# Kernel optimization log

Hardware: AMD Instinct MI355X
Metric: run time of the kernel (lower is better)

Reference implementation:

```python
import jax, jax.numpy as jnp
import numpy as np

DIM = 2048
NUM_EXPERTS = 64
TOP_K = 2


def setup_inputs() -> dict:
    key = jax.random.key(0)
    kx, kw = jax.random.split(key)
    x = jax.random.normal(kx, (4, 8192, DIM), dtype=jnp.float32)
    # nn.Linear(dim, num_experts, bias=False) -> weight [num_experts, dim]
    W = jax.random.normal(kw, (NUM_EXPERTS, DIM), dtype=jnp.float32) * (1.0 / np.sqrt(DIM))
    return {"x": x, "W": W}


def reference(x, W):
    # gate scores: [B, S, E]
    gate_scores = jnp.einsum("bsd,ed->bse", x, W)
    # top-k over experts
    top_k_values, top_k_indices = jax.lax.top_k(gate_scores, TOP_K)
    top_k_weights = jax.nn.softmax(top_k_values, axis=-1)  # [B, S, K]
    # load-balancing aux loss
    expert_usage = jax.nn.softmax(gate_scores, axis=-1).mean(axis=(0, 1))  # [E]
    aux_loss = NUM_EXPERTS * jnp.sum(expert_usage ** 2)
    return (top_k_indices, top_k_weights, aux_loss)
```

## Files before the change

kernel.cpp:

```cpp
#include <hip/hip_runtime.h>
#include <stdint.h>

#define DIM    2048
#define NE     64
#define NTOK   32768
#define BM     64
#define NTHR   512
#define BK     64
#define NIT    (DIM/BK)
#define WPLANE (NE*DIM)
#define S      68
#define ABUF   24576

typedef __attribute__((ext_vector_type(8)))  short  short8;
typedef __attribute__((ext_vector_type(16))) float  f32x16;

union U4S8 { uint4 u; short8 s; };

__device__ __forceinline__ unsigned pack_hi16(unsigned e0, unsigned e1) {
    return __builtin_amdgcn_perm(e1, e0, 0x07060302u);
}

__device__ __forceinline__ void split8(const float4& a, const float4& b,
                                       short8& h, short8& m, short8& l) {
    const float f[8] = {a.x, a.y, a.z, a.w, b.x, b.y, b.z, b.w};
    unsigned hb[8], mb[8], lb[8];
#pragma unroll
    for (int j = 0; j < 8; ++j) {
        const unsigned xb = __float_as_uint(f[j]);
        const unsigned th = xb & 0xffff0000u;
        const float    rh = f[j] - __uint_as_float(th);
        const unsigned rb = __float_as_uint(rh);
        const unsigned tm = rb & 0xffff0000u;
        const float    rm = rh - __uint_as_float(tm);
        hb[j] = th; mb[j] = tm; lb[j] = __float_as_uint(rm);
    }
    U4S8 H, M, L;
    H.u = make_uint4(pack_hi16(hb[0],hb[1]), pack_hi16(hb[2],hb[3]),
                     pack_hi16(hb[4],hb[5]), pack_hi16(hb[6],hb[7]));
    M.u = make_uint4(pack_hi16(mb[0],mb[1]), pack_hi16(mb[2],mb[3]),
                     pack_hi16(mb[4],mb[5]), pack_hi16(mb[6],mb[7]));
    L.u = make_uint4(pack_hi16(lb[0],lb[1]), pack_hi16(lb[2],lb[3]),
                     pack_hi16(lb[4],lb[5]), pack_hi16(lb[6],lb[7]));
    h = H.s; m = M.s; l = L.s;
}

__global__ void router_wsplit(const float* __restrict__ W, unsigned short* __restrict__ W3)
{
    const int i = blockIdx.x * 256 + threadIdx.x;
    const int e = i >> 11, k = i & 2047;
    const float f = W[i];
    const unsigned xb = __float_as_uint(f);
    const unsigned th = xb & 0xffff0000u;
    const float    rh = f - __uint_as_float(th);
    const unsigned rb = __float_as_uint(rh);
    const unsigned tm = rb & 0xffff0000u;
    const float    rm = rh - __uint_as_float(tm);
    const int dst = (k >> 4) * 1024 + e * 16 + (k & 15);
    W3[dst]            = (unsigned short)(th >> 16);
    W3[WPLANE + dst]   = (unsigned short)(tm >> 16);
    W3[2*WPLANE + dst] = (unsigned short)(__float_as_uint(rm) >> 16);
}

#define MFMA(A, B, C) __builtin_amdgcn_mfma_f32_32x32x16_bf16(A, B, C, 0, 0, 0)

__global__ __launch_bounds__(NTHR, 4)
void router_main(const float* __restrict__ x, const unsigned short* __restrict__ W3,
                 float* __restrict__ out_idx, float* __restrict__ out_w,
                 float* __restrict__ gusage)
{
    __shared__ __align__(16) unsigned char smem[2 * ABUF];

    const int tid  = threadIdx.x;
    const int w    = tid >> 6;
    const int ln   = tid & 63;
    const int wn   = w & 1;
    const int wkk  = w >> 1;
    const int tok0 = blockIdx.x * BM;
    const int arow = ln & 31;
    const int kh   = ln >> 5;

    const int xr = tid >> 3, xq = tid & 7;
    const float* xp = x + (size_t)(tok0 + xr) * DIM + xq * 8;
    const uint32_t awb = (uint32_t)(xr * 384 + ((xq ^ (xr & 7)) * 16));

    const uint32_t bvo = (uint32_t)((wkk * 1024 + wn * 512 + arow * 16 + kh * 8) * 2);

    const int aq = wkk * 2 + kh;
    const uint32_t arb = (uint32_t)(arow * 384 + ((aq ^ (arow & 7)) * 16));

    f32x16 acc[2];
#pragma unroll
    for (int mt = 0; mt < 2; ++mt)
#pragma unroll
        for (int r = 0; r < 16; ++r) acc[mt][r] = 0.f;

    float4 xa = *(const float4*)(xp);
    float4 xb = *(const float4*)(xp + 4);
    {
        short8 sh, sm, sl;
        split8(xa, xb, sh, sm, sl);
        *(short8*)(smem + awb)       = sh;
        *(short8*)(smem + awb + 128) = sm;
        *(short8*)(smem + awb + 256) = sl;
    }
    xa = *(const float4*)(xp + BK);
    xb = *(const float4*)(xp + BK + 4);
    U4S8 b0, b1, b2;
    b0.u = *(const uint4*)((const unsigned char*)W3 + bvo);
    b1.u = *(const uint4*)((const unsigned char*)W3 + bvo + 2*WPLANE);
    b2.u = *(const uint4*)((const unsigned char*)W3 + bvo + 4*WPLANE);
    __syncthreads();

#pragma unroll 2
    for (int kt = 0; kt < NIT; ++kt) {
        const uint32_t cb = (uint32_t)(kt & 1) * ABUF;
        const uint32_t nb = ABUF - cb;

        U4S8 n0, n1, n2;
        if (kt + 1 < NIT) {
            const uint32_t off = bvo + (uint32_t)(kt + 1) * 8192;
            n0.u = *(const uint4*)((const unsigned char*)W3 + off);
            n1.u = *(const uint4*)((const unsigned char*)W3 + off + 2*WPLANE);
            n2.u = *(const uint4*)((const unsigned char*)W3 + off + 4*WPLANE);
        }

        if (kt + 1 < NIT) {
            short8 sh, sm, sl;
            split8(xa, xb, sh, sm, sl);
            *(short8*)(smem + nb + awb)       = sh;
            *(short8*)(smem + nb + awb + 128) = sm;
            *(short8*)(smem + nb + awb + 256) = sl;
            if (kt + 2 < NIT) {
                xa = *(const float4*)(xp + (kt + 2) * BK);
                xb = *(const float4*)(xp + (kt + 2) * BK + 4);
            }
        }

#pragma unroll
        for (int mt = 0; mt < 2; ++mt) {
            const unsigned char* base = smem + cb + arb + mt * 12288;
            const short8 ah = *(const short8*)(base);
            const short8 am = *(const short8*)(base + 128);
            const short8 al = *(const short8*)(base + 256);
            acc[mt] = MFMA(ah, b0.s, acc[mt]);
            acc[mt] = MFMA(am, b0.s, acc[mt]);
            acc[mt] = MFMA(al, b0.s, acc[mt]);
            acc[mt] = MFMA(ah, b1.s, acc[mt]);
            acc[mt] = MFMA(am, b1.s, acc[mt]);
            acc[mt] = MFMA(ah, b2.s, acc[mt]);
        }
        b0 = n0; b1 = n1; b2 = n2;
        __syncthreads();
    }

    float* ps  = (float*)smem;
    float* mxa = (float*)(smem + 17408);
    float* zia = (float*)(smem + 17664);
    float* usa = (float*)(smem + 17920);

    for (int pass = 0; pass < 4; ++pass) {
        if (wkk == pass) {
#pragma unroll
            for (int mt = 0; mt < 2; ++mt)
#pragma unroll
                for (int r = 0; r < 16; ++r) {
                    const int t = mt*32 + (r & 3) + 8*(r >> 2) + 4*kh;
                    const int e = wn*32 + arow;
                    if (pass == 0) ps[t*S + e]  = acc[mt][r];
                    else           ps[t*S + e] += acc[mt][r];
                }
        }
        __syncthreads();
    }

    if (tid < BM) {
        const int t = tid;
        float v1 = -3.4e38f, v2 = -3.4e38f;
        int   i1 = 0, i2 = 0;
        for (int e = 0; e < NE; ++e) {
            float s = ps[t*S + e];
            if (s > v1)      { v2 = v1; i2 = i1; v1 = s; i1 = e; }
            else if (s > v2) { v2 = s;  i2 = e; }
        }
        float z = 0.f;
        for (int e = 0; e < NE; ++e) z += __expf(ps[t*S + e] - v1);
        mxa[t] = v1;
        zia[t] = 1.f / z;

        const int gt = tok0 + t;
        out_idx[gt*2 + 0] = (float)i1;
        out_idx[gt*2 + 1] = (float)i2;
        float e21 = __expf(v2 - v1);
        float w1  = 1.f / (1.f + e21);
        out_w[gt*2 + 0] = w1;
        out_w[gt*2 + 1] = e21 * w1;
    }
    __syncthreads();

    {
        const int e = tid & 63;
        const int c = tid >> 6;
        float u = 0.f;
        for (int t = c*8; t < c*8 + 8; ++t)
            u += __expf(ps[t*S + e] - mxa[t]) * zia[t];
        usa[c*64 + e] = u;
    }
    __syncthreads();
    if (tid < NE) {
        float u = 0.f;
#pragma unroll
        for (int c = 0; c < 8; ++c) u += usa[c*64 + tid];
        atomicAdd(&gusage[tid], u);
    }
}

__global__ void router_finalize(const float* __restrict__ gusage, float* __restrict__ out_aux)
{
    const int e = threadIdx.x;
    float u = gusage[e] * (1.0f / (float)NTOK);
    float s = u * u;
#pragma unroll
    for (int off = 32; off > 0; off >>= 1)
        s += __shfl_down(s, off, 64);
    if (e == 0) out_aux[0] = (float)NE * s;
}

extern "C" void kernel_launch(void* const* d_in, const int* in_sizes, int n_in,
                              void* d_out, int out_size, void* d_ws, size_t ws_size,
                              hipStream_t stream)
{
    const float* x = (const float*)d_in[0];
    const float* W = (const float*)d_in[1];
    float* out     = (float*)d_out;
    float* out_idx = out;
    float* out_w   = out + NTOK * 2;
    float* out_aux = out + NTOK * 4;

    unsigned short* W3 = (unsigned short*)d_ws;
    float* gusage = (float*)((char*)d_ws + 3 * WPLANE * sizeof(unsigned short));

    hipMemsetAsync(gusage, 0, NE * sizeof(float), stream);
    hipLaunchKernelGGL(router_wsplit, dim3(WPLANE / 256), dim3(256), 0, stream, W, W3);
    hipLaunchKernelGGL(router_main, dim3(NTOK / BM), dim3(NTHR), 0, stream,
                       x, W3, out_idx, out_w, gusage);
    hipLaunchKernelGGL(router_finalize, dim3(1), dim3(NE), 0, stream, gusage, out_aux);
}
```

Baseline: 377.9 us.

## Halve token tile to 32 rows with 256 threads, each wave covering two K-blocks

```diff
diff --git a/kernel.cpp b/kernel.cpp
--- a/kernel.cpp
+++ b/kernel.cpp
@@ -4,13 +4,13 @@
 #define DIM    2048
 #define NE     64
 #define NTOK   32768
-#define BM     64
-#define NTHR   512
+#define BM     32
+#define NTHR   256
 #define BK     64
 #define NIT    (DIM/BK)
 #define WPLANE (NE*DIM)
 #define S      68
-#define ABUF   24576
+#define ABUF   12288
 
 typedef __attribute__((ext_vector_type(8)))  short  short8;
 typedef __attribute__((ext_vector_type(16))) float  f32x16;
@@ -84,16 +84,21 @@
     const float* xp = x + (size_t)(tok0 + xr) * DIM + xq * 8;
     const uint32_t awb = (uint32_t)(xr * 384 + ((xq ^ (xr & 7)) * 16));
 
-    const uint32_t bvo = (uint32_t)((wkk * 1024 + wn * 512 + arow * 16 + kh * 8) * 2);
-
-    const int aq = wkk * 2 + kh;
-    const uint32_t arb = (uint32_t)(arow * 384 + ((aq ^ (arow & 7)) * 16));
-
-    f32x16 acc[2];
-#pragma unroll
-    for (int mt = 0; mt < 2; ++mt)
-#pragma unroll
-        for (int r = 0; r < 16; ++r) acc[mt][r] = 0.f;
+    uint32_t bvo[2];
+#pragma unroll
+    for (int kb = 0; kb < 2; ++kb)
+        bvo[kb] = (uint32_t)((((wkk*2 + kb) * 1024) + wn * 512 + arow * 16 + kh * 8) * 2);
+
+    uint32_t arb[2];
+#pragma unroll
+    for (int kb = 0; kb < 2; ++kb) {
+        const int q = wkk * 4 + kb * 2 + kh;
+        arb[kb] = (uint32_t)(arow * 384 + ((q ^ (arow & 7)) * 16));
+    }
+
+    f32x16 acc;
+#pragma unroll
+    for (int r = 0; r < 16; ++r) acc[r] = 0.f;
 
     float4 xa = *(const float4*)(xp);
     float4 xb = *(const float4*)(xp + 4);
@@ -106,10 +111,12 @@
     }
     xa = *(const float4*)(xp + BK);
     xb = *(const float4*)(xp + BK + 4);
-    U4S8 b0, b1, b2;
-    b0.u = *(const uint4*)((const unsigned char*)W3 + bvo);
-    b1.u = *(const uint4*)((const unsigned char*)W3 + bvo + 2*WPLANE);
-    b2.u = *(const uint4*)((const unsigned char*)W3 + bvo + 4*WPLANE);
+    U4S8 b[2][3];
+#pragma unroll
+    for (int kb = 0; kb < 2; ++kb)
+#pragma unroll
+        for (int p = 0; p < 3; ++p)
+            b[kb][p].u = *(const uint4*)((const unsigned char*)W3 + bvo[kb] + p * (2*WPLANE));
     __syncthreads();
 
 #pragma unroll 2
@@ -117,12 +124,19 @@
         const uint32_t cb = (uint32_t)(kt & 1) * ABUF;
         const uint32_t nb = ABUF - cb;
 
-        U4S8 n0, n1, n2;
+        float4 na, nc;
+        if (kt + 2 < NIT) {
+            na = *(const float4*)(xp + (kt + 2) * BK);
+            nc = *(const float4*)(xp + (kt + 2) * BK + 4);
+        }
+        U4S8 n[2][3];
         if (kt + 1 < NIT) {
-            const uint32_t off = bvo + (uint32_t)(kt + 1) * 8192;
-            n0.u = *(const uint4*)((const unsigned char*)W3 + off);
-            n1.u = *(const uint4*)((const unsigned char*)W3 + off + 2*WPLANE);
-            n2.u = *(const uint4*)((const unsigned char*)W3 + off + 4*WPLANE);
+            const uint32_t off = (uint32_t)(kt + 1) * 8192;
+#pragma unroll
+            for (int kb = 0; kb < 2; ++kb)
+#pragma unroll
+                for (int p = 0; p < 3; ++p)
+                    n[kb][p].u = *(const uint4*)((const unsigned char*)W3 + bvo[kb] + off + p * (2*WPLANE));
         }
 
         if (kt + 1 < NIT) {
@@ -131,45 +145,43 @@
             *(short8*)(smem + nb + awb)       = sh;
             *(short8*)(smem + nb + awb + 128) = sm;
             *(short8*)(smem + nb + awb + 256) = sl;
-            if (kt + 2 < NIT) {
-                xa = *(const float4*)(xp + (kt + 2) * BK);
-                xb = *(const float4*)(xp + (kt + 2) * BK + 4);
-            }
-        }
-
-#pragma unroll
-        for (int mt = 0; mt < 2; ++mt) {
-            const unsigned char* base = smem + cb + arb + mt * 12288;
+        }
+
+#pragma unroll
+        for (int kb = 0; kb < 2; ++kb) {
+            const unsigned char* base = smem + cb + arb[kb];
             const short8 ah = *(const short8*)(base);
             const short8 am = *(const short8*)(base + 128);
             const short8 al = *(const short8*)(base + 256);
-            acc[mt] = MFMA(ah, b0.s, acc[mt]);
-            acc[mt] = MFMA(am, b0.s, acc[mt]);
-            acc[mt] = MFMA(al, b0.s, acc[mt]);
-            acc[mt] = MFMA(ah, b1.s, acc[mt]);
-            acc[mt] = MFMA(am, b1.s, acc[mt]);
-            acc[mt] = MFMA(ah, b2.s, acc[mt]);
-        }
-        b0 = n0; b1 = n1; b2 = n2;
+            acc = MFMA(ah, b[kb][0].s, acc);
+            acc = MFMA(am, b[kb][0].s, acc);
+            acc = MFMA(al, b[kb][0].s, acc);
+            acc = MFMA(ah, b[kb][1].s, acc);
+            acc = MFMA(am, b[kb][1].s, acc);
+            acc = MFMA(ah, b[kb][2].s, acc);
+        }
+        xa = na; xb = nc;
+#pragma unroll
+        for (int kb = 0; kb < 2; ++kb)
+#pragma unroll
+            for (int p = 0; p < 3; ++p) b[kb][p] = n[kb][p];
         __syncthreads();
     }
 
     float* ps  = (float*)smem;
-    float* mxa = (float*)(smem + 17408);
-    float* zia = (float*)(smem + 17664);
-    float* usa = (float*)(smem + 17920);
-
-    for (int pass = 0; pass < 4; ++pass) {
+    float* mxa = (float*)(smem + 8704);
+    float* zia = (float*)(smem + 8832);
+    float* usa = (float*)(smem + 8960);
+
+    for (int pass = 0; pass < 2; ++pass) {
         if (wkk == pass) {
 #pragma unroll
-            for (int mt = 0; mt < 2; ++mt)
-#pragma unroll
-                for (int r = 0; r < 16; ++r) {
-                    const int t = mt*32 + (r & 3) + 8*(r >> 2) + 4*kh;
-                    const int e = wn*32 + arow;
-                    if (pass == 0) ps[t*S + e]  = acc[mt][r];
-                    else           ps[t*S + e] += acc[mt][r];
-                }
+            for (int r = 0; r < 16; ++r) {
+                const int t = (r & 3) + 8*(r >> 2) + 4*kh;
+                const int e = wn*32 + arow;
+                if (pass == 0) ps[t*S + e]  = acc[r];
+                else           ps[t*S + e] += acc[r];
+            }
         }
         __syncthreads();
     }
@@ -210,7 +222,7 @@
     if (tid < NE) {
         float u = 0.f;
 #pragma unroll
-        for (int c = 0; c < 8; ++c) u += usa[c*64 + tid];
+        for (int c = 0; c < 4; ++c) u += usa[c*64 + tid];
         atomicAdd(&gusage[tid], u);
     }
 }
```

Measured after the change: 382.4 us. About the same (+1.2%).
